# Kernel tuning notes

Measured on AMD Instinct MI355X. Metric: run time of the kernel, lower is better.

Reference implementation:

```python
import jax, jax.numpy as jnp
import numpy as np

B, S, EMB, H = 2, 2048, 1024, 16
D = EMB // H  # per-head dim = 64
SCALE = 1.0 / np.sqrt(D).astype(np.float32)


def setup_inputs() -> dict:
    key = jax.random.key(0)
    ks = jax.random.split(key, 11)
    lim = 1.0 / np.sqrt(EMB).astype(np.float32)  # torch Linear default init range
    def lin(kw, kb):
        W = jax.random.uniform(kw, (EMB, EMB), jnp.float32, -lim, lim)
        b = jax.random.uniform(kb, (EMB,), jnp.float32, -lim, lim)
        return W, b
    Wq, bq = lin(ks[0], ks[1])
    Wk, bk = lin(ks[2], ks[3])
    Wv, bv = lin(ks[4], ks[5])
    Wo, bo = lin(ks[6], ks[7])
    xq = jax.random.normal(ks[8], (B, S, EMB), jnp.float32)
    xk = jax.random.normal(ks[9], (B, S, EMB), jnp.float32)
    xv = jax.random.normal(ks[10], (B, S, EMB), jnp.float32)
    mask = jnp.tril(jnp.ones((S, S), dtype=jnp.int32))  # causal mask; 0 -> blocked
    return {"xq": xq, "xk": xk, "xv": xv, "mask": mask,
            "Wq": Wq, "bq": bq, "Wk": Wk, "bk": bk,
            "Wv": Wv, "bv": bv, "Wo": Wo, "bo": bo}


def reference(xq, xk, xv, mask, Wq, bq, Wk, bk, Wv, bv, Wo, bo):
    # Projections (torch Linear: x @ W.T + b), then split heads: [B,S,E] -> [B,H,S,D]
    def split_heads(x):
        return x.reshape(B, S, H, D).transpose(0, 2, 1, 3)
    Q = split_heads(xq @ Wq.T + bq)
    K = split_heads(xk @ Wk.T + bk)
    V = split_heads(xv @ Wv.T + bv)
    scores = jnp.einsum("bhqd,bhkd->bhqk", Q, K) * SCALE  # [B,H,S,S]
    scores = jnp.where(mask[None, None, :, :] == 0, jnp.float32(-1e9), scores)
    attn = jax.nn.softmax(scores, axis=-1)  # softmax over key axis (dim=2 per-head in torch)
    res = jnp.einsum("bhqk,bhkd->bhqd", attn, V)
    res = res.transpose(0, 2, 1, 3).reshape(B, S, EMB)  # merge heads back (same slicing layout)
    return res @ Wo.T + bo
```

## Files before the change

kernel.cpp:

```cpp
#include <hip/hip_runtime.h>
#include <hip/hip_bf16.h>

#define BB   2
#define SS   2048
#define EMBD 1024
#define NH   16
#define HD   64
#define QSCALE 0.18033688011112042f
#define NEG_BIG (-1e30f)

typedef __bf16 bf16;
typedef float  floatx4 __attribute__((ext_vector_type(4)));
typedef __bf16 bf16x4  __attribute__((ext_vector_type(4)));
typedef __bf16 bf16x8  __attribute__((ext_vector_type(8)));

typedef const __attribute__((address_space(1))) void* gas_ptr;
typedef __attribute__((address_space(3))) void*       las_ptr;

__device__ __forceinline__ void gl_lds16(const void* g, void* l) {
    __builtin_amdgcn_global_load_lds((gas_ptr)g, (las_ptr)l, 16, 0, 0);
}

__device__ __forceinline__ bf16x8 cvt8(const float* p) {
    bf16x8 o;
#pragma unroll
    for (int j = 0; j < 8; j++) o[j] = (bf16)p[j];
    return o;
}

__global__ __launch_bounds__(256) void cvt_all(
    const float* __restrict__ xq, const float* __restrict__ xk,
    const float* __restrict__ xv, const float* __restrict__ Wq,
    const float* __restrict__ Wk, const float* __restrict__ Wv,
    const float* __restrict__ Wo, bf16* __restrict__ xqo,
    bf16* __restrict__ xko, bf16* __restrict__ xvo, bf16* __restrict__ Wqo,
    bf16* __restrict__ Wko, bf16* __restrict__ Wvo, bf16* __restrict__ Woo) {
    const int y = blockIdx.y;
    const float* src;
    bf16* dst;
    size_t n;
    const size_t NX = (size_t)BB * SS * EMBD;
    const size_t NW = (size_t)EMBD * EMBD;
    switch (y) {
        case 0: src = xq; dst = xqo; n = NX; break;
        case 1: src = xk; dst = xko; n = NX; break;
        case 2: src = xv; dst = xvo; n = NX; break;
        case 3: src = Wq; dst = Wqo; n = NW; break;
        case 4: src = Wk; dst = Wko; n = NW; break;
        case 5: src = Wv; dst = Wvo; n = NW; break;
        default: src = Wo; dst = Woo; n = NW; break;
    }
    const size_t stride = (size_t)gridDim.x * blockDim.x * 4;
    for (size_t i = ((size_t)blockIdx.x * blockDim.x + threadIdx.x) * 4;
         i < n; i += stride) {
        floatx4 v = *(const floatx4*)(src + i);
        bf16x4 o = {(bf16)v[0], (bf16)v[1], (bf16)v[2], (bf16)v[3]};
        *(bf16x4*)(dst + i) = o;
    }
}

extern __shared__ __align__(16) char smem[];

template <int MODE, int FM>
__device__ __forceinline__ void gemm_body(const bf16* __restrict__ A,
                                          const bf16* __restrict__ W,
                                          const float* __restrict__ bias,
                                          void* __restrict__ Ov,
                                          int mBase, int nBase, float oscale) {
    constexpr int BM = 32 * FM;
    constexpr int ABYTES = BM * 64 * 2;
    bf16* As = (bf16*)smem;
    bf16* Bs = (bf16*)(smem + ABYTES);

    const int t = threadIdx.x;
    const int l = t & 63, w = t >> 6;
    const int lm = l & 15, lq = l >> 4;
    const int K = 1024;
    const int wm = (w >> 1) * (16 * FM), wn = (w & 1) * 64;

    const floatx4 zero = {0.f, 0.f, 0.f, 0.f};
    floatx4 acc[FM][4];
#pragma unroll
    for (int i = 0; i < FM; i++)
#pragma unroll
        for (int j = 0; j < 4; j++) acc[i][j] = zero;

    for (int kb = 0; kb < K; kb += 64) {
        __syncthreads();
#pragma unroll
        for (int ia = 0; ia < FM; ia++) {
            int half = ia / (FM / 2 > 0 ? FM / 2 : 1);
            int rem  = (ia % (FM / 2 > 0 ? FM / 2 : 1)) * 256 + t;
            int row  = rem >> 2;
            int col  = half * 32 + (rem & 3) * 8;
            gl_lds16(A + (size_t)(mBase + row) * K + kb + col,
                     (char*)As + (ia * 256 + w * 64) * 16);
        }
#pragma unroll
        for (int i = 0; i < 4; i++) {
            int half = i >> 1;
            int rem  = (i & 1) * 256 + t;
            int row  = rem >> 2;
            int col  = half * 32 + (rem & 3) * 8;
            gl_lds16(W + (size_t)(nBase + row) * K + kb + col,
                     (char*)Bs + (i * 256 + w * 64) * 16);
        }
        __syncthreads();

#pragma unroll
        for (int half = 0; half < 2; half++) {
            const bf16* Ah = As + half * BM * 32;
            const bf16* Bh = Bs + half * 128 * 32;
            bf16x8 af[FM], bfv[4];
#pragma unroll
            for (int f = 0; f < FM; f++)
                af[f] = *(const bf16x8*)&Ah[(wm + f * 16 + lm) * 32 + lq * 8];
#pragma unroll
            for (int f = 0; f < 4; f++)
                bfv[f] = *(const bf16x8*)&Bh[(wn + f * 16 + lm) * 32 + lq * 8];
            if (MODE == 2) {
#pragma unroll
                for (int i = 0; i < 4; i++)
#pragma unroll
                    for (int j = 0; j < FM; j++)
                        acc[j][i] = __builtin_amdgcn_mfma_f32_16x16x32_bf16(
                            bfv[i], af[j], acc[j][i], 0, 0, 0);
            } else {
#pragma unroll
                for (int fm = 0; fm < FM; fm++)
#pragma unroll
                    for (int fn = 0; fn < 4; fn++)
                        acc[fm][fn] =
                            __builtin_amdgcn_mfma_f32_16x16x32_bf16(
                                af[fm], bfv[fn], acc[fm][fn], 0, 0, 0);
            }
        }
    }

    __syncthreads();
    float* rp = (float*)smem + w * (16 * 68);

    if (MODE != 2) {
        float bvv[4];
#pragma unroll
        for (int fn = 0; fn < 4; fn++)
            bvv[fn] = bias[nBase + wn + fn * 16 + lm];
#pragma unroll
        for (int fm = 0; fm < FM; fm++) {
#pragma unroll
            for (int fn = 0; fn < 4; fn++)
#pragma unroll
                for (int r = 0; r < 4; r++)
                    rp[(lq * 4 + r) * 68 + fn * 16 + lm] =
                        (acc[fm][fn][r] + bvv[fn]) * oscale;
            if (MODE == 0) {
                int row2 = l >> 3, col8 = l & 7;
                int h = (nBase + wn) >> 6;
#pragma unroll
                for (int p = 0; p < 2; p++) {
                    int row = p * 8 + row2;
                    int m = mBase + wm + fm * 16 + row;
                    int b = m >> 11, s = m & 2047;
                    bf16x8 o = cvt8(&rp[row * 68 + col8 * 8]);
                    *(bf16x8*)((bf16*)Ov +
                               (((size_t)(b * NH + h)) * SS + s) * HD +
                               col8 * 8) = o;
                }
            } else {
                int c4 = l & 15;
#pragma unroll
                for (int p = 0; p < 4; p++) {
                    int row = p * 4 + (l >> 4);
                    int m = mBase + wm + fm * 16 + row;
                    floatx4 o = *(const floatx4*)&rp[row * 68 + c4 * 4];
                    *(floatx4*)((float*)Ov + (size_t)m * EMBD + nBase + wn +
                                c4 * 4) = o;
                }
            }
        }
    } else {
        const int b = (mBase + wm) >> 11;
        const int sbase = (mBase + wm) & 2047;
#pragma unroll
        for (int i = 0; i < 4; i++) {
            float bv[4];
#pragma unroll
            for (int r = 0; r < 4; r++)
                bv[r] = bias[nBase + wn + i * 16 + lq * 4 + r];
#pragma unroll
            for (int j = 0; j < FM; j++)
#pragma unroll
                for (int r = 0; r < 4; r++)
                    rp[(lq * 4 + r) * 68 + j * 16 + lm] =
                        acc[j][i][r] + bv[r];
            int row2 = l >> 3, col8 = l & 7;
#pragma unroll
            for (int p = 0; p < 2; p++) {
                int row = p * 8 + row2;
                int n = nBase + wn + i * 16 + row;
                int h = n >> 6, d = n & 63;
                bf16x8 o = cvt8(&rp[row * 68 + col8 * 8]);
                *(bf16x8*)((bf16*)Ov +
                           ((size_t)(b * NH + h) * HD + d) * SS + sbase +
                           col8 * 8) = o;
            }
        }
    }
}

__global__ __launch_bounds__(256, 4) void gemm_qkv(
    const bf16* __restrict__ xq, const bf16* __restrict__ xk,
    const bf16* __restrict__ xv, const bf16* __restrict__ Wq,
    const bf16* __restrict__ Wk, const bf16* __restrict__ Wv,
    const float* __restrict__ bq, const float* __restrict__ bk,
    const float* __restrict__ bv, bf16* __restrict__ Qo,
    bf16* __restrict__ Ko, bf16* __restrict__ Vo) {
    const int z = blockIdx.z;
    const int mB = blockIdx.x * 128, nB = blockIdx.y * 128;
    if (z == 0)
        gemm_body<0, 4>(xq, Wq, bq, Qo, mB, nB, QSCALE);
    else if (z == 1)
        gemm_body<0, 4>(xk, Wk, bk, Ko, mB, nB, 1.0f);
    else
        gemm_body<2, 4>(xv, Wv, bv, Vo, mB, nB, 1.0f);
}

__global__ __launch_bounds__(256, 4) void gemm_out(
    const bf16* __restrict__ A, const bf16* __restrict__ W,
    const float* __restrict__ bias, float* __restrict__ O) {
    gemm_body<1, 2>(A, W, bias, O, blockIdx.x * 64, blockIdx.y * 128, 1.0f);
}

__global__ __launch_bounds__(256, 3) void attn_fwd(
    const bf16* __restrict__ Qg, const bf16* __restrict__ Kg,
    const bf16* __restrict__ Vtg, bf16* __restrict__ Oatt) {
    __shared__ __align__(16) bf16 Ks[128 * 64];
    __shared__ __align__(16) bf16 VT[64 * 128];
    __shared__ __align__(16) bf16 Ps[4][16 * 64];

    const int t = threadIdx.x;
    const int l = t & 63, w = t >> 6;
    const int lm = l & 15, lq = l >> 4;
    const int m7 = lm & 7;
    const int x = blockIdx.x;
    const int i5 = x >> 5;
    const int gq = i5 >> 3, jq = i5 & 7;
    const int qt = (gq == 0) ? jq
                 : (gq == 1) ? 15 - jq
                 : (gq == 2) ? 16 + jq
                             : 31 - jq;
    const int bh = (((x >> 3) & 3) << 3) | (x & 7);
    const int nch = (qt >> 1) + 1;
    const size_t kbase = (size_t)bh * SS * HD;
    const size_t vbase = (size_t)bh * HD * SS;
    const int b = bh >> 4, h = bh & 15;
    const floatx4 zero = {0.f, 0.f, 0.f, 0.f};

    bf16x8 qa0, qa1;
    {
        const bf16* qp =
            Qg + kbase + (size_t)(qt * 64 + w * 16 + lm) * HD + lq * 8;
        qa0 = *(const bf16x8*)qp;
        qa1 = *(const bf16x8*)(qp + 32);
    }

    float m_i = NEG_BIG, l_i = 0.f;
    floatx4 od[4];
#pragma unroll
    for (int dt = 0; dt < 4; dt++) od[dt] = zero;

    const int qglob = qt * 64 + w * 16 + lm;

    bf16x8 kreg[4], vreg[4];
#pragma unroll
    for (int i = 0; i < 4; i++) {
        int idx = i * 256 + t;
        int rowK = idx >> 3, colK = (idx & 7) * 8;
        kreg[i] = *(const bf16x8*)(Kg + kbase + (size_t)rowK * HD + colK);
        int dV = idx >> 4, keyb = (idx & 15) * 8;
        vreg[i] = *(const bf16x8*)(Vtg + vbase + (size_t)dV * SS + keyb);
    }

    for (int kt = 0; kt < nch; ++kt) {
        __syncthreads();
#pragma unroll
        for (int i = 0; i < 4; i++) {
            int idx = i * 256 + t;
            int rowK = idx >> 3, c16 = idx & 7;
            *(bf16x8*)&Ks[rowK * 64 + ((c16 ^ (rowK & 7)) << 3)] = kreg[i];
            int dV = idx >> 4, k16 = idx & 15;
            *(bf16x8*)&VT[dV * 128 +
                          (((k16 & 8) | ((k16 ^ dV) & 7)) << 3)] = vreg[i];
        }
        __syncthreads();
        if (kt < nch - 1) {
#pragma unroll
            for (int i = 0; i < 4; i++) {
                int idx = i * 256 + t;
                int rowK = idx >> 3, colK = (idx & 7) * 8;
                kreg[i] = *(const bf16x8*)(
                    Kg + kbase + (size_t)((kt + 1) * 128 + rowK) * HD + colK);
                int dV = idx >> 4, keyb = (idx & 15) * 8;
                vreg[i] = *(const bf16x8*)(
                    Vtg + vbase + (size_t)dV * SS + (kt + 1) * 128 + keyb);
            }
        }

        floatx4 sc[8];
#pragma unroll
        for (int j0 = 0; j0 < 8; j0++) {
            int rowK = j0 * 16 + lm;
            bf16x8 k0 = *(const bf16x8*)&Ks[rowK * 64 + ((lq ^ m7) << 3)];
            bf16x8 k1 =
                *(const bf16x8*)&Ks[rowK * 64 + (((4 + lq) ^ m7) << 3)];
            floatx4 z = zero;
            z = __builtin_amdgcn_mfma_f32_16x16x32_bf16(k0, qa0, z, 0, 0, 0);
            z = __builtin_amdgcn_mfma_f32_16x16x32_bf16(k1, qa1, z, 0, 0, 0);
            sc[j0] = z;
        }
        if (kt == nch - 1) {
#pragma unroll
            for (int j0 = 0; j0 < 8; j0++)
#pragma unroll
                for (int r = 0; r < 4; r++) {
                    int key = kt * 128 + j0 * 16 + lq * 4 + r;
                    if (key > qglob) sc[j0][r] = NEG_BIG;
                }
        }
        float m4[4];
#pragma unroll
        for (int a = 0; a < 4; a++) {
            float u0 = fmaxf(fmaxf(sc[a][0], sc[a][1]),
                             fmaxf(sc[a][2], sc[a][3]));
            float u1 = fmaxf(fmaxf(sc[a + 4][0], sc[a + 4][1]),
                             fmaxf(sc[a + 4][2], sc[a + 4][3]));
            m4[a] = fmaxf(u0, u1);
        }
        float mt = fmaxf(fmaxf(m4[0], m4[1]), fmaxf(m4[2], m4[3]));
        mt = fmaxf(mt, __shfl_xor(mt, 16));
        mt = fmaxf(mt, __shfl_xor(mt, 32));
        float mnew = fmaxf(m_i, mt);
        float alpha = __builtin_amdgcn_exp2f(m_i - mnew);
        m_i = mnew;
        float psa0 = 0.f, psa1 = 0.f, psa2 = 0.f, psa3 = 0.f;
#pragma unroll
        for (int j0 = 0; j0 < 8; j0++) {
            float p0 = __builtin_amdgcn_exp2f(sc[j0][0] - mnew);
            float p1 = __builtin_amdgcn_exp2f(sc[j0][1] - mnew);
            float p2 = __builtin_amdgcn_exp2f(sc[j0][2] - mnew);
            float p3 = __builtin_amdgcn_exp2f(sc[j0][3] - mnew);
            sc[j0][0] = p0; sc[j0][1] = p1;
            sc[j0][2] = p2; sc[j0][3] = p3;
            psa0 += p0; psa1 += p1; psa2 += p2; psa3 += p3;
        }
        float ps = (psa0 + psa1) + (psa2 + psa3);
        ps += __shfl_xor(ps, 16);
        ps += __shfl_xor(ps, 32);
        l_i = l_i * alpha + ps;
        float a0 = __shfl(alpha, lq * 4 + 0);
        float a1 = __shfl(alpha, lq * 4 + 1);
        float a2 = __shfl(alpha, lq * 4 + 2);
        float a3 = __shfl(alpha, lq * 4 + 3);
#pragma unroll
        for (int dt = 0; dt < 4; dt++) {
            od[dt][0] *= a0;
            od[dt][1] *= a1;
            od[dt][2] *= a2;
            od[dt][3] *= a3;
        }
#pragma unroll
        for (int hv = 0; hv < 2; hv++) {
#pragma unroll
            for (int j0l = 0; j0l < 4; j0l++) {
                floatx4 s4 = sc[hv * 4 + j0l];
                bf16x4 pk = {(bf16)s4[0], (bf16)s4[1], (bf16)s4[2],
                             (bf16)s4[3]};
                *(bf16x4*)&Ps[w][lm * 64 +
                                 ((j0l * 16 + lq * 4) ^ (m7 * 8))] = pk;
            }
            bf16x8 pa0 =
                *(const bf16x8*)&Ps[w][lm * 64 + ((lq * 8) ^ (m7 * 8))];
            bf16x8 pa1 =
                *(const bf16x8*)&Ps[w][lm * 64 + ((32 + lq * 8) ^ (m7 * 8))];
#pragma unroll
            for (int dt = 0; dt < 4; dt++) {
                int rowD = dt * 16 + lm;
                int sl0 = hv * 8 + lq;
                int sl1 = sl0 + 4;
                bf16x8 v0 = *(const bf16x8*)&VT[
                    rowD * 128 + (((sl0 & 8) | ((sl0 ^ m7) & 7)) << 3)];
                od[dt] = __builtin_amdgcn_mfma_f32_16x16x32_bf16(pa0, v0,
                                                                 od[dt], 0, 0,
                                                                 0);
                bf16x8 v1 = *(const bf16x8*)&VT[
                    rowD * 128 + (((sl1 & 8) | ((sl1 ^ m7) & 7)) << 3)];
                od[dt] = __builtin_amdgcn_mfma_f32_16x16x32_bf16(pa1, v1,
                                                                 od[dt], 0, 0,
                                                                 0);
            }
        }
    }

    float linv = 1.0f / l_i;
    float lr0 = __shfl(linv, lq * 4 + 0);
    float lr1 = __shfl(linv, lq * 4 + 1);
    float lr2 = __shfl(linv, lq * 4 + 2);
    float lr3 = __shfl(linv, lq * 4 + 3);
    float lr[4] = {lr0, lr1, lr2, lr3};
#pragma unroll
    for (int dt = 0; dt < 4; dt++) {
#pragma unroll
        for (int r = 0; r < 4; r++) {
            int s = qt * 64 + w * 16 + lq * 4 + r;
            float v = od[dt][r] * lr[r];
            Oatt[((size_t)(b * SS + s)) * EMBD + h * HD + dt * 16 + lm] =
                (bf16)v;
        }
    }
}

extern "C" void kernel_launch(void* const* d_in, const int* in_sizes, int n_in,
                              void* d_out, int out_size, void* d_ws,
                              size_t ws_size, hipStream_t stream) {
    const float* xq = (const float*)d_in[0];
    const float* xk = (const float*)d_in[1];
    const float* xv = (const float*)d_in[2];
    const float* Wq = (const float*)d_in[4];
    const float* bq = (const float*)d_in[5];
    const float* Wk = (const float*)d_in[6];
    const float* bk = (const float*)d_in[7];
    const float* Wv = (const float*)d_in[8];
    const float* bv = (const float*)d_in[9];
    const float* Wo = (const float*)d_in[10];
    const float* bo = (const float*)d_in[11];
    float* out = (float*)d_out;

    const size_t NX = (size_t)BB * SS * EMBD;
    const size_t NW = (size_t)EMBD * EMBD;
    bf16* Qw  = (bf16*)d_ws;
    bf16* Kw  = Qw + NX;
    bf16* Vw  = Kw + NX;
    bf16* Aw  = Vw + NX;
    bf16* xqb = Aw + NX;
    bf16* xkb = xqb + NX;
    bf16* xvb = xkb + NX;
    bf16* Wqb = xvb + NX;
    bf16* Wkb = Wqb + NW;
    bf16* Wvb = Wkb + NW;
    bf16* Wob = Wvb + NW;

    cvt_all<<<dim3(1024, 7), 256, 0, stream>>>(xq, xk, xv, Wq, Wk, Wv, Wo,
                                               xqb, xkb, xvb, Wqb, Wkb, Wvb,
                                               Wob);
    gemm_qkv<<<dim3(32, 8, 3), 256, 32768, stream>>>(
        xqb, xkb, xvb, Wqb, Wkb, Wvb, bq, bk, bv, Qw, Kw, Vw);
    attn_fwd<<<dim3(1024), 256, 0, stream>>>(Qw, Kw, Vw, Aw);
    gemm_out<<<dim3(64, 8), 256, 24576, stream>>>(Aw, Wob, bo, out);
}
```

Before: 229.2 us.

## Double-buffer 64-key K/V tiles in LDS via direct global-to-LDS loads

The attention loop now walks 64-key chunks instead of 128-key chunks. Each chunk is loaded straight into LDS with global_load_lds into a double buffer, replacing register staging plus a manual LDS store. The loads for the next chunk are issued before computing the current one, and each iteration needs only one barrier instead of two. The smaller chunks also skip masked work past the causal diagonal at 64-key granularity. In exchange there are twice as many iterations, each with less MFMA work, so softmax rescaling overhead per key goes up.

Result: faster. 224.1 us (-2.2%).

```diff
diff --git a/kernel.cpp b/kernel.cpp
--- a/kernel.cpp
+++ b/kernel.cpp
@@ -234,8 +234,8 @@
 __global__ __launch_bounds__(256, 3) void attn_fwd(
     const bf16* __restrict__ Qg, const bf16* __restrict__ Kg,
     const bf16* __restrict__ Vtg, bf16* __restrict__ Oatt) {
-    __shared__ __align__(16) bf16 Ks[128 * 64];
-    __shared__ __align__(16) bf16 VT[64 * 128];
+    __shared__ __align__(16) bf16 Ksb[2 * 64 * 64];
+    __shared__ __align__(16) bf16 VTb[2 * 64 * 64];
     __shared__ __align__(16) bf16 Ps[4][16 * 64];
 
     const int t = threadIdx.x;
@@ -250,11 +250,17 @@
                  : (gq == 2) ? 16 + jq
                              : 31 - jq;
     const int bh = (((x >> 3) & 3) << 3) | (x & 7);
-    const int nch = (qt >> 1) + 1;
     const size_t kbase = (size_t)bh * SS * HD;
     const size_t vbase = (size_t)bh * HD * SS;
     const int b = bh >> 4, h = bh & 15;
     const floatx4 zero = {0.f, 0.f, 0.f, 0.f};
+
+    const int trow = t >> 3, tsl = t & 7;
+    const int cswz = ((tsl ^ (trow & 7)) << 3);
+    const bf16* kgp = Kg + kbase + (size_t)trow * HD + cswz;
+    const bf16* vgp = Vtg + vbase + (size_t)trow * SS + cswz;
+    bf16* ksd = Ksb + t * 8;
+    bf16* vtd = VTb + t * 8;
 
     bf16x8 qa0, qa1;
     {
@@ -271,71 +277,53 @@
 
     const int qglob = qt * 64 + w * 16 + lm;
 
-    bf16x8 kreg[4], vreg[4];
-#pragma unroll
-    for (int i = 0; i < 4; i++) {
-        int idx = i * 256 + t;
-        int rowK = idx >> 3, colK = (idx & 7) * 8;
-        kreg[i] = *(const bf16x8*)(Kg + kbase + (size_t)rowK * HD + colK);
-        int dV = idx >> 4, keyb = (idx & 15) * 8;
-        vreg[i] = *(const bf16x8*)(Vtg + vbase + (size_t)dV * SS + keyb);
-    }
-
-    for (int kt = 0; kt < nch; ++kt) {
-        __syncthreads();
-#pragma unroll
-        for (int i = 0; i < 4; i++) {
-            int idx = i * 256 + t;
-            int rowK = idx >> 3, c16 = idx & 7;
-            *(bf16x8*)&Ks[rowK * 64 + ((c16 ^ (rowK & 7)) << 3)] = kreg[i];
-            int dV = idx >> 4, k16 = idx & 15;
-            *(bf16x8*)&VT[dV * 128 +
-                          (((k16 & 8) | ((k16 ^ dV) & 7)) << 3)] = vreg[i];
-        }
-        __syncthreads();
-        if (kt < nch - 1) {
-#pragma unroll
-            for (int i = 0; i < 4; i++) {
-                int idx = i * 256 + t;
-                int rowK = idx >> 3, colK = (idx & 7) * 8;
-                kreg[i] = *(const bf16x8*)(
-                    Kg + kbase + (size_t)((kt + 1) * 128 + rowK) * HD + colK);
-                int dV = idx >> 4, keyb = (idx & 15) * 8;
-                vreg[i] = *(const bf16x8*)(
-                    Vtg + vbase + (size_t)dV * SS + (kt + 1) * 128 + keyb);
-            }
-        }
-
-        floatx4 sc[8];
-#pragma unroll
-        for (int j0 = 0; j0 < 8; j0++) {
+    gl_lds16(kgp, ksd);
+    gl_lds16(kgp + 2048, ksd + 2048);
+    gl_lds16(vgp, vtd);
+    gl_lds16(vgp + 32 * SS, vtd + 2048);
+    __syncthreads();
+
+    for (int kt = 0; kt <= qt; ++kt) {
+        const int cur = kt & 1;
+        const bf16* Kc = Ksb + cur * 4096;
+        const bf16* Vc = VTb + cur * 4096;
+        if (kt < qt) {
+            const bf16* kp = kgp + (size_t)(kt + 1) * 4096;
+            const bf16* vp = vgp + (size_t)(kt + 1) * 64;
+            bf16* kn = ksd + (cur ^ 1) * 4096;
+            bf16* vn = vtd + (cur ^ 1) * 4096;
+            gl_lds16(kp, kn);
+            gl_lds16(kp + 2048, kn + 2048);
+            gl_lds16(vp, vn);
+            gl_lds16(vp + 32 * SS, vn + 2048);
+        }
+
+        floatx4 sc[4];
+#pragma unroll
+        for (int j0 = 0; j0 < 4; j0++) {
             int rowK = j0 * 16 + lm;
-            bf16x8 k0 = *(const bf16x8*)&Ks[rowK * 64 + ((lq ^ m7) << 3)];
+            bf16x8 k0 = *(const bf16x8*)&Kc[rowK * 64 + ((lq ^ m7) << 3)];
             bf16x8 k1 =
-                *(const bf16x8*)&Ks[rowK * 64 + (((4 + lq) ^ m7) << 3)];
+                *(const bf16x8*)&Kc[rowK * 64 + (((4 + lq) ^ m7) << 3)];
             floatx4 z = zero;
             z = __builtin_amdgcn_mfma_f32_16x16x32_bf16(k0, qa0, z, 0, 0, 0);
             z = __builtin_amdgcn_mfma_f32_16x16x32_bf16(k1, qa1, z, 0, 0, 0);
             sc[j0] = z;
         }
-        if (kt == nch - 1) {
-#pragma unroll
-            for (int j0 = 0; j0 < 8; j0++)
+        if (kt == qt) {
+#pragma unroll
+            for (int j0 = 0; j0 < 4; j0++)
 #pragma unroll
                 for (int r = 0; r < 4; r++) {
-                    int key = kt * 128 + j0 * 16 + lq * 4 + r;
+                    int key = kt * 64 + j0 * 16 + lq * 4 + r;
                     if (key > qglob) sc[j0][r] = NEG_BIG;
                 }
         }
         float m4[4];
 #pragma unroll
-        for (int a = 0; a < 4; a++) {
-            float u0 = fmaxf(fmaxf(sc[a][0], sc[a][1]),
-                             fmaxf(sc[a][2], sc[a][3]));
-            float u1 = fmaxf(fmaxf(sc[a + 4][0], sc[a + 4][1]),
-                             fmaxf(sc[a + 4][2], sc[a + 4][3]));
-            m4[a] = fmaxf(u0, u1);
-        }
+        for (int a = 0; a < 4; a++)
+            m4[a] = fmaxf(fmaxf(sc[a][0], sc[a][1]),
+                          fmaxf(sc[a][2], sc[a][3]));
         float mt = fmaxf(fmaxf(m4[0], m4[1]), fmaxf(m4[2], m4[3]));
         mt = fmaxf(mt, __shfl_xor(mt, 16));
         mt = fmaxf(mt, __shfl_xor(mt, 32));
@@ -344,7 +332,7 @@
         m_i = mnew;
         float psa0 = 0.f, psa1 = 0.f, psa2 = 0.f, psa3 = 0.f;
 #pragma unroll
-        for (int j0 = 0; j0 < 8; j0++) {
+        for (int j0 = 0; j0 < 4; j0++) {
             float p0 = __builtin_amdgcn_exp2f(sc[j0][0] - mnew);
             float p1 = __builtin_amdgcn_exp2f(sc[j0][1] - mnew);
             float p2 = __builtin_amdgcn_exp2f(sc[j0][2] - mnew);
@@ -369,36 +357,26 @@
             od[dt][3] *= a3;
         }
 #pragma unroll
-        for (int hv = 0; hv < 2; hv++) {
-#pragma unroll
-            for (int j0l = 0; j0l < 4; j0l++) {
-                floatx4 s4 = sc[hv * 4 + j0l];
-                bf16x4 pk = {(bf16)s4[0], (bf16)s4[1], (bf16)s4[2],
-                             (bf16)s4[3]};
-                *(bf16x4*)&Ps[w][lm * 64 +
-                                 ((j0l * 16 + lq * 4) ^ (m7 * 8))] = pk;
-            }
-            bf16x8 pa0 =
-                *(const bf16x8*)&Ps[w][lm * 64 + ((lq * 8) ^ (m7 * 8))];
-            bf16x8 pa1 =
-                *(const bf16x8*)&Ps[w][lm * 64 + ((32 + lq * 8) ^ (m7 * 8))];
-#pragma unroll
-            for (int dt = 0; dt < 4; dt++) {
-                int rowD = dt * 16 + lm;
-                int sl0 = hv * 8 + lq;
-                int sl1 = sl0 + 4;
-                bf16x8 v0 = *(const bf16x8*)&VT[
-                    rowD * 128 + (((sl0 & 8) | ((sl0 ^ m7) & 7)) << 3)];
-                od[dt] = __builtin_amdgcn_mfma_f32_16x16x32_bf16(pa0, v0,
-                                                                 od[dt], 0, 0,
-                                                                 0);
-                bf16x8 v1 = *(const bf16x8*)&VT[
-                    rowD * 128 + (((sl1 & 8) | ((sl1 ^ m7) & 7)) << 3)];
-                od[dt] = __builtin_amdgcn_mfma_f32_16x16x32_bf16(pa1, v1,
-                                                                 od[dt], 0, 0,
-                                                                 0);
-            }
-        }
+        for (int j0l = 0; j0l < 4; j0l++) {
+            floatx4 s4 = sc[j0l];
+            bf16x4 pk = {(bf16)s4[0], (bf16)s4[1], (bf16)s4[2], (bf16)s4[3]};
+            *(bf16x4*)&Ps[w][lm * 64 + ((j0l * 16 + lq * 4) ^ (m7 * 8))] = pk;
+        }
+        bf16x8 pa0 = *(const bf16x8*)&Ps[w][lm * 64 + ((lq * 8) ^ (m7 * 8))];
+        bf16x8 pa1 =
+            *(const bf16x8*)&Ps[w][lm * 64 + ((32 + lq * 8) ^ (m7 * 8))];
+#pragma unroll
+        for (int dt = 0; dt < 4; dt++) {
+            int rowD = dt * 16 + lm;
+            bf16x8 v0 = *(const bf16x8*)&Vc[rowD * 64 + ((lq ^ m7) << 3)];
+            od[dt] = __builtin_amdgcn_mfma_f32_16x16x32_bf16(pa0, v0, od[dt],
+                                                             0, 0, 0);
+            bf16x8 v1 =
+                *(const bf16x8*)&Vc[rowD * 64 + (((4 + lq) ^ m7) << 3)];
+            od[dt] = __builtin_amdgcn_mfma_f32_16x16x32_bf16(pa1, v1, od[dt],
+                                                             0, 0, 0);
+        }
+        __syncthreads();
     }
 
     float linv = 1.0f / l_i;
```
